# Kernel optimization log

Measured on AMD Instinct MI355X. Metric: run time of the kernel, lower is better.

The kernel has to match this reference:

```python
import jax, jax.numpy as jnp
import numpy as np

# Forest of complete L-ary trees, BFS level-contiguous node numbering.
B_TREES, ARITY, DEPTH = 8, 4, 8
C, M, NGEN = 8, 100, 4
COUNTS = [B_TREES * ARITY**l for l in range(DEPTH + 1)]
OFFS = np.concatenate([[0], np.cumsum(COUNTS)]).astype(np.int64)
DIM = int(OFFS[-1])  # 699048
# tree id of each node: within-level index // (ARITY**level)
BATCH = np.concatenate([np.arange(COUNTS[l]) // (ARITY**l) for l in range(DEPTH + 1)])


def setup_inputs() -> dict:
    key = jax.random.key(0)
    k1, k2, k3, k4 = jax.random.split(key, 4)
    return {
        "x": jax.random.randint(k1, (DIM,), 0, M, dtype=jnp.int32),
        "A": jax.random.normal(k2, (C, C, ARITY, NGEN), dtype=jnp.float32) * 2.5,
        "B_emit": jax.random.normal(k3, (C, M, NGEN), dtype=jnp.float32) * 2.5,
        "Pi": jax.random.normal(k4, (C, NGEN), dtype=jnp.float32) * 2.5,
    }


def _htmm_loglik(x, A, B_emit, Pi):
    # softmax reparameterization (matches F.softmax axes in torch code)
    smA = jax.nn.softmax(A, axis=0)            # [C,C,L,G], over child state
    smA_t = jnp.transpose(smA, (2, 0, 1, 3))   # [L,C,C,G]
    smB = jax.nn.softmax(B_emit, axis=1)       # [C,M,G]
    smPi = jax.nn.softmax(Pi, axis=0)          # [C,G]

    # preliminary downward: prior state distribution per node, level by level.
    # Children of a parent are contiguous with sibling position j = idx % ARITY.
    prior_lvls = [jnp.broadcast_to(smPi, (COUNTS[0], C, NGEN))]
    for l in range(1, DEPTH + 1):
        n_pa = COUNTS[l - 1]
        # prior_child[c] = sum_d A[c, d, pos_j, g] * prior_pa[d]
        pl = jnp.einsum('jcdg,pdg->pjcg', smA_t, prior_lvls[-1])
        prior_lvls.append(pl.reshape(n_pa * ARITY, C, NGEN))
    prior = jnp.concatenate(prior_lvls, axis=0)  # [DIM,C,G]

    em = jnp.transpose(smB[:, x], (1, 0, 2))     # [DIM,C,G]
    beta0 = prior * em

    ll = jnp.zeros((DIM, NGEN), dtype=beta0.dtype)
    # leaves = deepest level
    beta_lvl = beta0[OFFS[DEPTH]:OFFS[DEPTH + 1]]
    nu = beta_lvl.sum(1)                          # [n_leaves,G]
    beta_lvl = beta_lvl / nu[:, None, :]
    ll = ll.at[OFFS[DEPTH]:OFFS[DEPTH + 1]].set(jnp.log(nu))

    # upward recursion, bottom-up
    for l in range(DEPTH, 0, -1):
        n_pa = COUNTS[l - 1]
        ratio = (beta_lvl / prior[OFFS[l]:OFFS[l + 1]]).reshape(n_pa, ARITY, C, NGEN)
        # beta_uv[d] = sum_c A[c, d, pos_j, g] * beta_ch[c] / prior_ch[c]
        beta_uv = jnp.einsum('jcdg,pjcg->pjdg', smA_t, ratio)  # [n_pa,L,C,G]
        beta_pa = beta0[OFFS[l - 1]:OFFS[l]] * jnp.prod(beta_uv, axis=1)
        nu = beta_pa.sum(1)
        beta_lvl = beta_pa / nu[:, None, :]
        ll = ll.at[OFFS[l - 1]:OFFS[l]].set(jnp.log(nu))

    # scatter per-node log-likelihood contributions into per-tree totals
    return jax.ops.segment_sum(ll, jnp.asarray(BATCH), num_segments=B_TREES)  # [B_TREES,G]


def reference(x, A, B_emit, Pi):
    return _htmm_loglik(x, A, B_emit, Pi)
```

## Files before the change

### kernel.cpp

```cpp
#include <hip/hip_runtime.h>

constexpr int OFFS1 = 8, OFFS2 = 40, OFFS3 = 168, OFFS4 = 680;
constexpr int OFFS5 = 2728, OFFS6 = 10920, OFFS7 = 43688, OFFS8 = 174760;


#define WB() __builtin_amdgcn_wave_barrier()
#define AG_ST(p, v) __hip_atomic_store((p), (v), __ATOMIC_RELAXED, __HIP_MEMORY_SCOPE_AGENT)
#define AG_LD(p) __hip_atomic_load((p), __ATOMIC_RELAXED, __HIP_MEMORY_SCOPE_AGENT)

template <int CTRL>
static __device__ __forceinline__ float qadd(float v) {
  int x = __builtin_amdgcn_update_dpp(0, __float_as_int(v), CTRL, 0xF, 0xF, true);
  return v + __int_as_float(x);
}
static __device__ __forceinline__ float bfly8(float v) {
  v = qadd<0xB1>(v);
  v = qadd<0x4E>(v);
  int x = __builtin_amdgcn_ds_swizzle(__float_as_int(v), 0x101F);
  return v + __int_as_float(x);
}

static __device__ __forceinline__ void ld8(const float* p, float pv[8]) {
  const float4* q = (const float4*)p;
  float4 a = q[0], b = q[1];
  pv[0] = a.x; pv[1] = a.y; pv[2] = a.z; pv[3] = a.w;
  pv[4] = b.x; pv[5] = b.y; pv[6] = b.z; pv[7] = b.w;
}

static __device__ __forceinline__ float dot8r(const float w[8], const float* p) {
  const float4* q = (const float4*)p;
  float4 a = q[0], b = q[1];
  return w[0] * a.x + w[1] * a.y + w[2] * a.z + w[3] * a.w +
         w[4] * b.x + w[5] * b.y + w[6] * b.z + w[7] * b.w;
}

static __device__ __forceinline__ float rcpf(float x) { return __builtin_amdgcn_rcpf(x); }

__global__ __launch_bounds__(256) void k_all(const int* __restrict__ x,
                                             const float* __restrict__ A,
                                             const float* __restrict__ Bm,
                                             const float* __restrict__ Pi,
                                             float* __restrict__ RAT4,
                                             float* __restrict__ blocksum,
                                             unsigned* __restrict__ ctr,
                                             float* __restrict__ out) {
  __shared__ __align__(16) float wtd_l[1024];
  __shared__ __align__(16) float emt_l[3200];
  __shared__ __align__(16) float pit_l[32];
  __shared__ __align__(16) float etab_l[12800];
  __shared__ __align__(16) float shbuf[2304];
  __shared__ __align__(16) float rat5buf[16][32];
  __shared__ __align__(16) float pri4buf[4][32];
  __shared__ float llb[4];
  __shared__ int lastf;

  int t = threadIdx.x;
  int r = t & 31, g = r >> 3, s = r & 7, grp = t >> 5;
  int b = blockIdx.x, tree = b >> 6;

  if (t < 128) {
    int d = t >> 4, j = (t >> 2) & 3, gg = t & 3;
    float v[8], sum = 0.f;
#pragma unroll
    for (int ss = 0; ss < 8; ss++) { v[ss] = __expf(A[((ss * 8 + d) * 4 + j) * 4 + gg]); sum += v[ss]; }
    float inv = rcpf(sum);
#pragma unroll
    for (int ss = 0; ss < 8; ss++) wtd_l[(j * 8 + d) * 32 + gg * 8 + ss] = v[ss] * inv;
  }
  if (t < 4) {
    float v[8], sum = 0.f;
#pragma unroll
    for (int c = 0; c < 8; c++) { v[c] = __expf(Pi[c * 4 + t]); sum += v[c]; }
    float inv = rcpf(sum);
#pragma unroll
    for (int c = 0; c < 8; c++) pit_l[t * 8 + c] = v[c] * inv;
    llb[t] = 0.f;
  }
  {
    int row = t >> 3, part = t & 7, c = row >> 2, gg = row & 3;
    int m0 = part < 4 ? part * 13 : 52 + (part - 4) * 12;
    int mn = part < 4 ? 13 : 12;
    float sum = 0.f;
    for (int m = m0; m < m0 + mn; m++) sum += __expf(Bm[(c * 100 + m) * 4 + gg]);
    sum = bfly8(sum);
    float inv = rcpf(sum);
    for (int m = m0; m < m0 + mn; m++)
      emt_l[m * 32 + gg * 8 + c] = __expf(Bm[(c * 100 + m) * 4 + gg]) * inv;
  }
  __syncthreads();
  {
    int c7 = t & 127, half = t >> 7;
    int j = c7 >> 5, d = (c7 >> 2) & 7, gg = c7 & 3;
    float w[8];
    ld8(&wtd_l[(j * 8 + d) * 32 + gg * 8], w);
    for (int m = half * 50; m < half * 50 + 50; m++)
      etab_l[(m * 4 + j) * 32 + gg * 8 + d] = dot8r(w, &emt_l[m * 32 + gg * 8]);
  }
  float wtd_r[4][8], wup_r[4][8];
#pragma unroll
  for (int j = 0; j < 4; j++) {
#pragma unroll
    for (int d = 0; d < 8; d++) wtd_r[j][d] = wtd_l[(j * 8 + d) * 32 + r];
    ld8(&wtd_l[(j * 8 + s) * 32 + g * 8], wup_r[j]);
  }
  __syncthreads();

  float* st = &shbuf[grp * 288];
  float acc = 0.f;
#pragma unroll 1
  for (int round = 0; round < 2; round++) {
    int n5 = b * 16 + round * 8 + grp;
    float v5 = pit_l[r], pri4 = 0.f;
#pragma unroll
    for (int k = 1; k <= 5; k++) {
      int j = (n5 >> (2 * (5 - k))) & 3;
      st[256 + r] = v5; WB();
      float pv[8]; ld8(st + 256 + g * 8, pv); WB();
      float nv = 0.f;
#pragma unroll
      for (int d = 0; d < 8; d++) nv += wtd_l[(j * 8 + d) * 32 + r] * pv[d];
      v5 = nv;
      if (k == 4) pri4 = v5;
    }
    float pv5[8];
    st[256 + r] = v5; WB(); ld8(st + 256 + g * 8, pv5); WB();

    const int4* x8v = (const int4*)(x + OFFS8 + n5 * 64);
    const int4* x7v = (const int4*)(x + OFFS7 + n5 * 16);
    int4 x6v = *(const int4*)(x + OFFS6 + n5 * 4);
    int x5s = x[OFFS5 + n5];
    const int* x6a = (const int*)&x6v;

#pragma unroll
    for (int q6 = 0; q6 < 4; q6++) {
      int4 x7 = x7v[q6];
      const int* x7a = (const int*)&x7;
      float u6 = 0.f;
#pragma unroll
      for (int d = 0; d < 8; d++) u6 += wtd_r[q6][d] * pv5[d];
      float pv6[8];
      st[256 + r] = u6; WB(); ld8(st + 256 + g * 8, pv6); WB();

      int4 xls[4];
      float Ep[4][4];
#pragma unroll
      for (int q7 = 0; q7 < 4; q7++) {
        xls[q7] = x8v[q6 * 4 + q7];
        const int* xla = (const int*)&xls[q7];
#pragma unroll
        for (int j = 0; j < 4; j++) Ep[q7][j] = etab_l[(xla[j] * 4 + j) * 32 + r];
      }

#pragma unroll
      for (int q7 = 0; q7 < 4; q7++) {
        float u7 = 0.f;
#pragma unroll
        for (int d = 0; d < 8; d++) u7 += wtd_r[q7][d] * pv6[d];
        float n0 = bfly8(u7 * Ep[q7][0]);
        float n1 = bfly8(u7 * Ep[q7][1]);
        float n2 = bfly8(u7 * Ep[q7][2]);
        float n3 = bfly8(u7 * Ep[q7][3]);
        float p01 = n0 * n1, p23 = n2 * n3;
        float prod = (Ep[q7][0] * Ep[q7][1] * rcpf(p01)) * (Ep[q7][2] * Ep[q7][3] * rcpf(p23));
        acc += __logf(p01) + __logf(p23);
        float em = emt_l[x7a[q7] * 32 + r];
        float nu7 = bfly8(u7 * em * prod);
        acc += __logf(nu7);
        st[q7 * 32 + r] = em * prod * rcpf(nu7);
      }
      WB();
      float prod6 = 1.f;
#pragma unroll
      for (int j = 0; j < 4; j++) prod6 *= dot8r(wup_r[j], st + j * 32 + g * 8);
      WB();
      float em6 = emt_l[x6a[q6] * 32 + r];
      float nu6 = bfly8(u6 * em6 * prod6);
      acc += __logf(nu6);
      st[(4 + q6) * 32 + r] = em6 * prod6 * rcpf(nu6);
    }
    WB();
    {
      float prod5 = 1.f;
#pragma unroll
      for (int j = 0; j < 4; j++) prod5 *= dot8r(wup_r[j], st + (4 + j) * 32 + g * 8);
      WB();
      float em5 = emt_l[x5s * 32 + r];
      float nu5 = bfly8(v5 * em5 * prod5);
      acc += __logf(nu5);
      rat5buf[round * 8 + grp][r] = em5 * prod5 * rcpf(nu5);
    }
    if ((grp & 3) == 0) pri4buf[round * 2 + (grp >> 2)][r] = pri4;
  }
  __syncthreads();

  if (grp < 4) {
    int n4 = b * 4 + grp;
    float prod = 1.f;
#pragma unroll
    for (int j = 0; j < 4; j++) prod *= dot8r(wup_r[j], &rat5buf[grp * 4 + j][g * 8]);
    float em = emt_l[x[OFFS4 + n4] * 32 + r];
    float pr4 = pri4buf[grp][r];
    float nu = bfly8(pr4 * em * prod);
    acc += __logf(nu);
    AG_ST(&RAT4[n4 * 32 + r], em * prod * rcpf(nu));
  }

  if (s == 0) atomicAdd(&llb[g], acc);
  __syncthreads();
  if (t < 4) AG_ST(&blocksum[b * 4 + t], llb[t]);
  asm volatile("s_waitcnt vmcnt(0)" ::: "memory");
  __syncthreads();
  if (t == 0) {
    unsigned old = __hip_atomic_fetch_add(&ctr[tree * 32], 1u, __ATOMIC_RELAXED,
                                          __HIP_MEMORY_SCOPE_AGENT);
    lastf = (old == 63u || old == 0xAAAAAAE9u) ? 1 : 0;
  }
  __syncthreads();
  if (!lastf) return;

  float* rat4_l = etab_l;
#pragma unroll
  for (int ib = 0; ib < 4; ib++) {
    float tmp[8];
#pragma unroll
    for (int i = 0; i < 8; i++) tmp[i] = AG_LD(&RAT4[tree * 8192 + (ib * 8 + i) * 256 + t]);
#pragma unroll
    for (int i = 0; i < 8; i++) rat4_l[(ib * 8 + i) * 256 + t] = tmp[i];
  }
  if (t < 4) llb[t] = 0.f;
  __syncthreads();

  float acc2 = 0.f;
#pragma unroll 1
  for (int ii = 0; ii < 2; ii++) {
    int l2 = ii * 8 + grp;
    int n2g = tree * 16 + l2;
    float v2 = pit_l[r];
#pragma unroll
    for (int k = 1; k <= 2; k++) {
      int j = (n2g >> (2 * (2 - k))) & 3;
      st[256 + r] = v2; WB();
      float pv[8]; ld8(st + 256 + g * 8, pv); WB();
      float nv = 0.f;
#pragma unroll
      for (int d = 0; d < 8; d++) nv += wtd_l[(j * 8 + d) * 32 + r] * pv[d];
      v2 = nv;
    }
    float pv2[8];
    st[256 + r] = v2; WB(); ld8(st + 256 + g * 8, pv2); WB();
#pragma unroll
    for (int j3 = 0; j3 < 4; j3++) {
      int n3g = n2g * 4 + j3;
      int i3l = l2 * 4 + j3;
      float p3 = 0.f;
#pragma unroll
      for (int d = 0; d < 8; d++) p3 += wtd_r[j3][d] * pv2[d];
      float prod = 1.f;
#pragma unroll
      for (int j = 0; j < 4; j++) prod *= dot8r(wup_r[j], &rat4_l[(i3l * 4 + j) * 32 + g * 8]);
      float em = emt_l[x[OFFS3 + n3g] * 32 + r];
      float nu = bfly8(p3 * em * prod);
      acc2 += __logf(nu);
      st[j3 * 32 + r] = em * prod * rcpf(nu);
    }
    WB();
    float prod = 1.f;
#pragma unroll
    for (int j = 0; j < 4; j++) prod *= dot8r(wup_r[j], st + j * 32 + g * 8);
    WB();
    float em = emt_l[x[OFFS2 + n2g] * 32 + r];
    float nu = bfly8(v2 * em * prod);
    acc2 += __logf(nu);
    st[(5 + ii) * 32 + r] = em * prod * rcpf(nu);
  }
  __syncthreads();
  if (grp < 4) {
    int n1g = tree * 4 + grp;
    float pv[8]; ld8(pit_l + g * 8, pv);
    float v1 = 0.f;
#pragma unroll
    for (int d = 0; d < 8; d++) v1 += wtd_l[(grp * 8 + d) * 32 + r] * pv[d];
    float prod = 1.f;
#pragma unroll
    for (int j = 0; j < 4; j++) {
      int l2 = grp * 4 + j;
      prod *= dot8r(wup_r[j], &shbuf[(l2 & 7) * 288 + (5 + (l2 >> 3)) * 32 + g * 8]);
    }
    float em = emt_l[x[OFFS1 + n1g] * 32 + r];
    float nu = bfly8(v1 * em * prod);
    acc2 += __logf(nu);
    st[7 * 32 + r] = em * prod * rcpf(nu);
  }
  __syncthreads();
  if (grp == 0) {
    float pr = pit_l[r];
    float prod = 1.f;
#pragma unroll
    for (int j = 0; j < 4; j++) prod *= dot8r(wup_r[j], &shbuf[j * 288 + 7 * 32 + g * 8]);
    float em = emt_l[x[tree] * 32 + r];
    float nu = bfly8(pr * em * prod);
    acc2 += __logf(nu);
  }
  __syncthreads();
  if (s == 0) atomicAdd(&llb[g], acc2);
  float v = AG_LD(&blocksum[tree * 256 + t]);
  __syncthreads();
  shbuf[t] = v;
  __syncthreads();
#pragma unroll
  for (int off = 128; off >= 4; off >>= 1) {
    if (t < off) shbuf[t] += shbuf[t + off];
    __syncthreads();
  }
  if (t < 4) out[tree * 4 + t] = shbuf[t] + llb[t];
}

extern "C" void kernel_launch(void* const* d_in, const int* in_sizes, int n_in,
                              void* d_out, int out_size, void* d_ws, size_t ws_size,
                              hipStream_t stream) {
  const int* x = (const int*)d_in[0];
  const float* A = (const float*)d_in[1];
  const float* Bm = (const float*)d_in[2];
  const float* Pi = (const float*)d_in[3];
  float* ws = (float*)d_ws;
  unsigned* ctr = (unsigned*)d_ws;
  float* blocksum = ws + 256;
  float* RAT4 = ws + 256 + 2048;
  float* out = (float*)d_out;

  k_all<<<512, 256, 0, stream>>>(x, A, Bm, Pi, RAT4, blocksum, ctr, out);
}
```

Measured before the change: 94.81 us.

## Use 512-thread blocks, DPP gathers for matvecs, and fp16 emission tables

Doubles the block size so each warp group handles one level-5 subtree instead of looping over two rounds. The shared-memory stage-and-reload for the 8-wide matrix-vector products is replaced with DPP lane gathers and branchless weight selection. Emission tables are stored as fp16 and all shared buffers are packed into one array, which cuts LDS use. The intent is fewer LDS round trips and wave barriers and better latency hiding, at the cost of fp16 precision on emission probabilities, more registers per thread, and a reworked last-block reduction.

```diff
diff --git a/kernel.cpp b/kernel.cpp
--- a/kernel.cpp
+++ b/kernel.cpp
@@ -9,34 +9,70 @@
 #define AG_LD(p) __hip_atomic_load((p), __ATOMIC_RELAXED, __HIP_MEMORY_SCOPE_AGENT)
 
 template <int CTRL>
-static __device__ __forceinline__ float qadd(float v) {
-  int x = __builtin_amdgcn_update_dpp(0, __float_as_int(v), CTRL, 0xF, 0xF, true);
-  return v + __int_as_float(x);
+static __device__ __forceinline__ float dppmov(float v) {
+  return __int_as_float(__builtin_amdgcn_update_dpp(0, __float_as_int(v), CTRL, 0xF, 0xF, true));
 }
 static __device__ __forceinline__ float bfly8(float v) {
-  v = qadd<0xB1>(v);
-  v = qadd<0x4E>(v);
-  int x = __builtin_amdgcn_ds_swizzle(__float_as_int(v), 0x101F);
-  return v + __int_as_float(x);
-}
-
+  v += dppmov<0xB1>(v);
+  v += dppmov<0x4E>(v);
+  v += dppmov<0x141>(v);
+  return v;
+}
+static __device__ __forceinline__ float red16(float v) {
+  v += dppmov<0xB1>(v);
+  v += dppmov<0x4E>(v);
+  v += dppmov<0x141>(v);
+  v += dppmov<0x140>(v);
+  return v;
+}
+constexpr int PX[8] = {0, 1, 2, 3, 7, 6, 5, 4};
+struct O8 { float a[8]; };
+static __device__ __forceinline__ O8 gather8(float v) {
+  O8 o;
+  o.a[0] = v;
+  o.a[1] = dppmov<0xB1>(v);
+  o.a[2] = dppmov<0x4E>(v);
+  o.a[3] = dppmov<0x1B>(v);
+  o.a[4] = dppmov<0x141>(v);
+  o.a[5] = dppmov<0x141>(o.a[1]);
+  o.a[6] = dppmov<0x141>(o.a[2]);
+  o.a[7] = dppmov<0x141>(o.a[3]);
+  return o;
+}
+static __device__ __forceinline__ float mvc(const float w[8], const O8& o) {
+  float acc = 0.f;
+#pragma unroll
+  for (int i = 0; i < 8; i++) acc += w[i] * o.a[i];
+  return acc;
+}
+static __device__ __forceinline__ float mv_sel(const float wq[4][8], const O8& o, int j) {
+  float acc = 0.f;
+#pragma unroll
+  for (int i = 0; i < 8; i++) {
+    float w01 = (j & 1) ? wq[1][i] : wq[0][i];
+    float w23 = (j & 1) ? wq[3][i] : wq[2][i];
+    float w = (j & 2) ? w23 : w01;
+    acc += w * o.a[i];
+  }
+  return acc;
+}
+static __device__ __forceinline__ float dot8r(const float w[8], const float* p) {
+  const float4* q = (const float4*)p;
+  float4 a = q[0], b = q[1];
+  return w[0] * a.x + w[1] * a.y + w[2] * a.z + w[3] * a.w +
+         w[4] * b.x + w[5] * b.y + w[6] * b.z + w[7] * b.w;
+}
 static __device__ __forceinline__ void ld8(const float* p, float pv[8]) {
   const float4* q = (const float4*)p;
   float4 a = q[0], b = q[1];
   pv[0] = a.x; pv[1] = a.y; pv[2] = a.z; pv[3] = a.w;
   pv[4] = b.x; pv[5] = b.y; pv[6] = b.z; pv[7] = b.w;
 }
-
-static __device__ __forceinline__ float dot8r(const float w[8], const float* p) {
-  const float4* q = (const float4*)p;
-  float4 a = q[0], b = q[1];
-  return w[0] * a.x + w[1] * a.y + w[2] * a.z + w[3] * a.w +
-         w[4] * b.x + w[5] * b.y + w[6] * b.z + w[7] * b.w;
-}
-
 static __device__ __forceinline__ float rcpf(float x) { return __builtin_amdgcn_rcpf(x); }
 
-__global__ __launch_bounds__(256) void k_all(const int* __restrict__ x,
+constexpr int SMEM_F = 19936;
+
+__global__ __launch_bounds__(512) void k_all(const int* __restrict__ x,
                                              const float* __restrict__ A,
                                              const float* __restrict__ Bm,
                                              const float* __restrict__ Pi,
@@ -44,15 +80,18 @@
                                              float* __restrict__ blocksum,
                                              unsigned* __restrict__ ctr,
                                              float* __restrict__ out) {
-  __shared__ __align__(16) float wtd_l[1024];
-  __shared__ __align__(16) float emt_l[3200];
-  __shared__ __align__(16) float pit_l[32];
-  __shared__ __align__(16) float etab_l[12800];
-  __shared__ __align__(16) float shbuf[2304];
-  __shared__ __align__(16) float rat5buf[16][32];
-  __shared__ __align__(16) float pri4buf[4][32];
+  __shared__ __align__(16) float smem[SMEM_F];
   __shared__ float llb[4];
   __shared__ int lastf;
+  float* wtd_l = smem;
+  float* pit_l = smem + 1024;
+  float* stash = smem + 1056;
+  float* rat5buf = smem + 3104;
+  float* pri4buf = smem + 3616;
+  float* emt_f = smem + 3744;
+  float* rat4_l = smem + 3744;
+  _Float16* emt_h = (_Float16*)(smem + 11936);
+  _Float16* etab_h = (_Float16*)(smem + 13536);
 
   int t = threadIdx.x;
   int r = t & 31, g = r >> 3, s = r & 7, grp = t >> 5;
@@ -77,130 +116,122 @@
     llb[t] = 0.f;
   }
   {
-    int row = t >> 3, part = t & 7, c = row >> 2, gg = row & 3;
-    int m0 = part < 4 ? part * 13 : 52 + (part - 4) * 12;
-    int mn = part < 4 ? 13 : 12;
+    int row = t >> 4, part = t & 15, c = row >> 2, gg = row & 3;
+    int m0 = part < 4 ? part * 7 : 28 + (part - 4) * 6;
+    int mn = part < 4 ? 7 : 6;
     float sum = 0.f;
     for (int m = m0; m < m0 + mn; m++) sum += __expf(Bm[(c * 100 + m) * 4 + gg]);
-    sum = bfly8(sum);
+    sum = red16(sum);
     float inv = rcpf(sum);
-    for (int m = m0; m < m0 + mn; m++)
-      emt_l[m * 32 + gg * 8 + c] = __expf(Bm[(c * 100 + m) * 4 + gg]) * inv;
-  }
-  __syncthreads();
-  {
-    int c7 = t & 127, half = t >> 7;
-    int j = c7 >> 5, d = (c7 >> 2) & 7, gg = c7 & 3;
-    float w[8];
-    ld8(&wtd_l[(j * 8 + d) * 32 + gg * 8], w);
-    for (int m = half * 50; m < half * 50 + 50; m++)
-      etab_l[(m * 4 + j) * 32 + gg * 8 + d] = dot8r(w, &emt_l[m * 32 + gg * 8]);
-  }
-  float wtd_r[4][8], wup_r[4][8];
+    for (int m = m0; m < m0 + mn; m++) {
+      float e = __expf(Bm[(c * 100 + m) * 4 + gg]) * inv;
+      emt_f[m * 32 + gg * 8 + c] = e;
+      emt_h[m * 32 + gg * 8 + c] = (_Float16)e;
+    }
+  }
+  __syncthreads();
+  {
+    int j = grp & 3, mq = grp >> 2;
+    float wu8[8];
+#pragma unroll
+    for (int i = 0; i < 8; i++) wu8[i] = wtd_l[(j * 8 + s) * 32 + g * 8 + (s ^ PX[i])];
+    for (int m = mq * 25; m < mq * 25 + 25; m++) {
+      O8 o = gather8(emt_f[m * 32 + r]);
+      etab_h[(m * 4 + j) * 32 + r] = (_Float16)mvc(wu8, o);
+    }
+  }
+  float wq[4][8], wup_r[4][8];
 #pragma unroll
   for (int j = 0; j < 4; j++) {
 #pragma unroll
-    for (int d = 0; d < 8; d++) wtd_r[j][d] = wtd_l[(j * 8 + d) * 32 + r];
+    for (int i = 0; i < 8; i++) wq[j][i] = wtd_l[(j * 8 + (s ^ PX[i])) * 32 + r];
     ld8(&wtd_l[(j * 8 + s) * 32 + g * 8], wup_r[j]);
   }
   __syncthreads();
 
-  float* st = &shbuf[grp * 288];
+  float* st = stash + grp * 128;
+  int n5 = b * 16 + grp;
   float acc = 0.f;
-#pragma unroll 1
-  for (int round = 0; round < 2; round++) {
-    int n5 = b * 16 + round * 8 + grp;
-    float v5 = pit_l[r], pri4 = 0.f;
-#pragma unroll
-    for (int k = 1; k <= 5; k++) {
-      int j = (n5 >> (2 * (5 - k))) & 3;
-      st[256 + r] = v5; WB();
-      float pv[8]; ld8(st + 256 + g * 8, pv); WB();
-      float nv = 0.f;
-#pragma unroll
-      for (int d = 0; d < 8; d++) nv += wtd_l[(j * 8 + d) * 32 + r] * pv[d];
-      v5 = nv;
-      if (k == 4) pri4 = v5;
-    }
-    float pv5[8];
-    st[256 + r] = v5; WB(); ld8(st + 256 + g * 8, pv5); WB();
-
-    const int4* x8v = (const int4*)(x + OFFS8 + n5 * 64);
-    const int4* x7v = (const int4*)(x + OFFS7 + n5 * 16);
-    int4 x6v = *(const int4*)(x + OFFS6 + n5 * 4);
-    int x5s = x[OFFS5 + n5];
-    const int* x6a = (const int*)&x6v;
-
-#pragma unroll
-    for (int q6 = 0; q6 < 4; q6++) {
-      int4 x7 = x7v[q6];
-      const int* x7a = (const int*)&x7;
-      float u6 = 0.f;
-#pragma unroll
-      for (int d = 0; d < 8; d++) u6 += wtd_r[q6][d] * pv5[d];
-      float pv6[8];
-      st[256 + r] = u6; WB(); ld8(st + 256 + g * 8, pv6); WB();
-
-      int4 xls[4];
-      float Ep[4][4];
-#pragma unroll
-      for (int q7 = 0; q7 < 4; q7++) {
-        xls[q7] = x8v[q6 * 4 + q7];
-        const int* xla = (const int*)&xls[q7];
-#pragma unroll
-        for (int j = 0; j < 4; j++) Ep[q7][j] = etab_l[(xla[j] * 4 + j) * 32 + r];
-      }
-
-#pragma unroll
-      for (int q7 = 0; q7 < 4; q7++) {
-        float u7 = 0.f;
-#pragma unroll
-        for (int d = 0; d < 8; d++) u7 += wtd_r[q7][d] * pv6[d];
-        float n0 = bfly8(u7 * Ep[q7][0]);
-        float n1 = bfly8(u7 * Ep[q7][1]);
-        float n2 = bfly8(u7 * Ep[q7][2]);
-        float n3 = bfly8(u7 * Ep[q7][3]);
-        float p01 = n0 * n1, p23 = n2 * n3;
-        float prod = (Ep[q7][0] * Ep[q7][1] * rcpf(p01)) * (Ep[q7][2] * Ep[q7][3] * rcpf(p23));
-        acc += __logf(p01) + __logf(p23);
-        float em = emt_l[x7a[q7] * 32 + r];
-        float nu7 = bfly8(u7 * em * prod);
-        acc += __logf(nu7);
-        st[q7 * 32 + r] = em * prod * rcpf(nu7);
-      }
-      WB();
-      float prod6 = 1.f;
-#pragma unroll
-      for (int j = 0; j < 4; j++) prod6 *= dot8r(wup_r[j], st + j * 32 + g * 8);
-      WB();
-      float em6 = emt_l[x6a[q6] * 32 + r];
-      float nu6 = bfly8(u6 * em6 * prod6);
-      acc += __logf(nu6);
-      st[(4 + q6) * 32 + r] = em6 * prod6 * rcpf(nu6);
+
+  float v = pit_l[r], pri4 = 0.f;
+#pragma unroll
+  for (int k = 1; k <= 5; k++) {
+    O8 o = gather8(v);
+    int j = (n5 >> (2 * (5 - k))) & 3;
+    v = mv_sel(wq, o, j);
+    if (k == 4) pri4 = v;
+  }
+  float v5 = v;
+  O8 o5 = gather8(v5);
+
+  const int4* x8v = (const int4*)(x + OFFS8 + n5 * 64);
+  const int4* x7v = (const int4*)(x + OFFS7 + n5 * 16);
+  int4 x6v = *(const int4*)(x + OFFS6 + n5 * 4);
+  int x5s = x[OFFS5 + n5];
+  const int* x6a = (const int*)&x6v;
+
+  float l6r[4];
+#pragma unroll
+  for (int q6 = 0; q6 < 4; q6++) {
+    int4 x7 = x7v[q6];
+    const int* x7a = (const int*)&x7;
+    float u6 = mvc(wq[q6], o5);
+    O8 o6 = gather8(u6);
+    float Ep[4][4];
+#pragma unroll
+    for (int q7 = 0; q7 < 4; q7++) {
+      int4 xl = x8v[q6 * 4 + q7];
+      const int* xla = (const int*)&xl;
+#pragma unroll
+      for (int j = 0; j < 4; j++) Ep[q7][j] = (float)etab_h[(xla[j] * 4 + j) * 32 + r];
+    }
+#pragma unroll
+    for (int q7 = 0; q7 < 4; q7++) {
+      float u7 = mvc(wq[q7], o6);
+      float n0 = bfly8(u7 * Ep[q7][0]);
+      float n1 = bfly8(u7 * Ep[q7][1]);
+      float n2 = bfly8(u7 * Ep[q7][2]);
+      float n3 = bfly8(u7 * Ep[q7][3]);
+      float p01 = n0 * n1, p23 = n2 * n3;
+      float prod = (Ep[q7][0] * Ep[q7][1] * rcpf(p01)) * (Ep[q7][2] * Ep[q7][3] * rcpf(p23));
+      acc += __logf(p01) + __logf(p23);
+      float em = (float)emt_h[x7a[q7] * 32 + r];
+      float nu7 = bfly8(u7 * em * prod);
+      acc += __logf(nu7);
+      st[q7 * 32 + r] = em * prod * rcpf(nu7);
     }
     WB();
-    {
-      float prod5 = 1.f;
-#pragma unroll
-      for (int j = 0; j < 4; j++) prod5 *= dot8r(wup_r[j], st + (4 + j) * 32 + g * 8);
-      WB();
-      float em5 = emt_l[x5s * 32 + r];
-      float nu5 = bfly8(v5 * em5 * prod5);
-      acc += __logf(nu5);
-      rat5buf[round * 8 + grp][r] = em5 * prod5 * rcpf(nu5);
-    }
-    if ((grp & 3) == 0) pri4buf[round * 2 + (grp >> 2)][r] = pri4;
-  }
+    float prod6 = 1.f;
+#pragma unroll
+    for (int j = 0; j < 4; j++) prod6 *= dot8r(wup_r[j], st + j * 32 + g * 8);
+    WB();
+    float em6 = (float)emt_h[x6a[q6] * 32 + r];
+    float nu6 = bfly8(u6 * em6 * prod6);
+    acc += __logf(nu6);
+    l6r[q6] = em6 * prod6 * rcpf(nu6);
+  }
+#pragma unroll
+  for (int j = 0; j < 4; j++) st[j * 32 + r] = l6r[j];
+  WB();
+  {
+    float prod5 = 1.f;
+#pragma unroll
+    for (int j = 0; j < 4; j++) prod5 *= dot8r(wup_r[j], st + j * 32 + g * 8);
+    float em5 = (float)emt_h[x5s * 32 + r];
+    float nu5 = bfly8(v5 * em5 * prod5);
+    acc += __logf(nu5);
+    rat5buf[grp * 32 + r] = em5 * prod5 * rcpf(nu5);
+  }
+  if ((grp & 3) == 0) pri4buf[(grp >> 2) * 32 + r] = pri4;
   __syncthreads();
 
   if (grp < 4) {
     int n4 = b * 4 + grp;
     float prod = 1.f;
 #pragma unroll
-    for (int j = 0; j < 4; j++) prod *= dot8r(wup_r[j], &rat5buf[grp * 4 + j][g * 8]);
-    float em = emt_l[x[OFFS4 + n4] * 32 + r];
-    float pr4 = pri4buf[grp][r];
-    float nu = bfly8(pr4 * em * prod);
+    for (int j = 0; j < 4; j++) prod *= dot8r(wup_r[j], &rat5buf[(grp * 4 + j) * 32 + g * 8]);
+    float em = (float)emt_h[x[OFFS4 + n4] * 32 + r];
+    float nu = bfly8(pri4buf[grp * 32 + r] * em * prod);
     acc += __logf(nu);
     AG_ST(&RAT4[n4 * 32 + r], em * prod * rcpf(nu));
   }
@@ -218,47 +249,36 @@
   __syncthreads();
   if (!lastf) return;
 
-  float* rat4_l = etab_l;
-#pragma unroll
-  for (int ib = 0; ib < 4; ib++) {
-    float tmp[8];
-#pragma unroll
-    for (int i = 0; i < 8; i++) tmp[i] = AG_LD(&RAT4[tree * 8192 + (ib * 8 + i) * 256 + t]);
-#pragma unroll
-    for (int i = 0; i < 8; i++) rat4_l[(ib * 8 + i) * 256 + t] = tmp[i];
-  }
   if (t < 4) llb[t] = 0.f;
+  {
+    float tmp[16];
+#pragma unroll
+    for (int i = 0; i < 16; i++) tmp[i] = AG_LD(&RAT4[tree * 8192 + i * 512 + t]);
+#pragma unroll
+    for (int i = 0; i < 16; i++) rat4_l[i * 512 + t] = tmp[i];
+  }
   __syncthreads();
 
   float acc2 = 0.f;
-#pragma unroll 1
-  for (int ii = 0; ii < 2; ii++) {
-    int l2 = ii * 8 + grp;
-    int n2g = tree * 16 + l2;
+  {
+    int n2g = tree * 16 + grp;
     float v2 = pit_l[r];
 #pragma unroll
     for (int k = 1; k <= 2; k++) {
+      O8 o = gather8(v2);
       int j = (n2g >> (2 * (2 - k))) & 3;
-      st[256 + r] = v2; WB();
-      float pv[8]; ld8(st + 256 + g * 8, pv); WB();
-      float nv = 0.f;
-#pragma unroll
-      for (int d = 0; d < 8; d++) nv += wtd_l[(j * 8 + d) * 32 + r] * pv[d];
-      v2 = nv;
-    }
-    float pv2[8];
-    st[256 + r] = v2; WB(); ld8(st + 256 + g * 8, pv2); WB();
+      v2 = mv_sel(wq, o, j);
+    }
+    O8 o2 = gather8(v2);
 #pragma unroll
     for (int j3 = 0; j3 < 4; j3++) {
       int n3g = n2g * 4 + j3;
-      int i3l = l2 * 4 + j3;
-      float p3 = 0.f;
-#pragma unroll
-      for (int d = 0; d < 8; d++) p3 += wtd_r[j3][d] * pv2[d];
+      int i3l = grp * 4 + j3;
+      float p3 = mvc(wq[j3], o2);
       float prod = 1.f;
 #pragma unroll
       for (int j = 0; j < 4; j++) prod *= dot8r(wup_r[j], &rat4_l[(i3l * 4 + j) * 32 + g * 8]);
-      float em = emt_l[x[OFFS3 + n3g] * 32 + r];
+      float em = (float)emt_h[x[OFFS3 + n3g] * 32 + r];
       float nu = bfly8(p3 * em * prod);
       acc2 += __logf(nu);
       st[j3 * 32 + r] = em * prod * rcpf(nu);
@@ -268,51 +288,44 @@
 #pragma unroll
     for (int j = 0; j < 4; j++) prod *= dot8r(wup_r[j], st + j * 32 + g * 8);
     WB();
-    float em = emt_l[x[OFFS2 + n2g] * 32 + r];
+    float em = (float)emt_h[x[OFFS2 + n2g] * 32 + r];
     float nu = bfly8(v2 * em * prod);
     acc2 += __logf(nu);
-    st[(5 + ii) * 32 + r] = em * prod * rcpf(nu);
+    rat5buf[grp * 32 + r] = em * prod * rcpf(nu);
   }
   __syncthreads();
   if (grp < 4) {
     int n1g = tree * 4 + grp;
-    float pv[8]; ld8(pit_l + g * 8, pv);
-    float v1 = 0.f;
-#pragma unroll
-    for (int d = 0; d < 8; d++) v1 += wtd_l[(grp * 8 + d) * 32 + r] * pv[d];
+    O8 op = gather8(pit_l[r]);
+    float v1 = mv_sel(wq, op, grp);
     float prod = 1.f;
 #pragma unroll
-    for (int j = 0; j < 4; j++) {
-      int l2 = grp * 4 + j;
-      prod *= dot8r(wup_r[j], &shbuf[(l2 & 7) * 288 + (5 + (l2 >> 3)) * 32 + g * 8]);
-    }
-    float em = emt_l[x[OFFS1 + n1g] * 32 + r];
+    for (int j = 0; j < 4; j++) prod *= dot8r(wup_r[j], &rat5buf[(grp * 4 + j) * 32 + g * 8]);
+    float em = (float)emt_h[x[OFFS1 + n1g] * 32 + r];
     float nu = bfly8(v1 * em * prod);
     acc2 += __logf(nu);
-    st[7 * 32 + r] = em * prod * rcpf(nu);
+    pri4buf[grp * 32 + r] = em * prod * rcpf(nu);
   }
   __syncthreads();
   if (grp == 0) {
-    float pr = pit_l[r];
     float prod = 1.f;
 #pragma unroll
-    for (int j = 0; j < 4; j++) prod *= dot8r(wup_r[j], &shbuf[j * 288 + 7 * 32 + g * 8]);
-    float em = emt_l[x[tree] * 32 + r];
-    float nu = bfly8(pr * em * prod);
+    for (int j = 0; j < 4; j++) prod *= dot8r(wup_r[j], &pri4buf[j * 32 + g * 8]);
+    float em = (float)emt_h[x[tree] * 32 + r];
+    float nu = bfly8(pit_l[r] * em * prod);
     acc2 += __logf(nu);
   }
-  __syncthreads();
   if (s == 0) atomicAdd(&llb[g], acc2);
-  float v = AG_LD(&blocksum[tree * 256 + t]);
-  __syncthreads();
-  shbuf[t] = v;
+  __syncthreads();
+  float* red = rat4_l;
+  if (t < 256) red[t] = AG_LD(&blocksum[tree * 256 + t]);
   __syncthreads();
 #pragma unroll
   for (int off = 128; off >= 4; off >>= 1) {
-    if (t < off) shbuf[t] += shbuf[t + off];
+    if (t < off) red[t] += red[t + off];
     __syncthreads();
   }
-  if (t < 4) out[tree * 4 + t] = shbuf[t] + llb[t];
+  if (t < 4) out[tree * 4 + t] = red[t] + llb[t];
 }
 
 extern "C" void kernel_launch(void* const* d_in, const int* in_sizes, int n_in,
@@ -328,5 +341,5 @@
   float* RAT4 = ws + 256 + 2048;
   float* out = (float*)d_out;
 
-  k_all<<<512, 256, 0, stream>>>(x, A, Bm, Pi, RAT4, blocksum, ctr, out);
-}
+  k_all<<<512, 512, 0, stream>>>(x, A, Bm, Pi, RAT4, blocksum, ctr, out);
+}
```

Result: slower. 108.0 us (+13.9%).
